# Kernel tuning notes

Measured on AMD Instinct MI355X. Metric: run time of the kernel, lower is better.

Reference implementation:

```python
import jax, jax.numpy as jnp
import numpy as np

EPS = 1e-8

def _div(a, b, eps=EPS):
    # torch: a / (b*(b>eps) + (b<=eps)*eps)
    return a / jnp.where(b > eps, b, eps)

def _cos_lastdim(a, b, eps=EPS):
    # F.cosine_similarity(a, b, dim=-1): dot / (max(|a|,eps)*max(|b|,eps))
    dot = jnp.sum(a * b, axis=-1)
    na = jnp.sqrt(jnp.sum(a * a, axis=-1))
    nb = jnp.sqrt(jnp.sum(b * b, axis=-1))
    return dot / (jnp.maximum(na, eps) * jnp.maximum(nb, eps))

def _full_matching(q1, q2, w):
    # q1,q2: [b,s,h]; w: [p,h] -> [b,s,p]
    q1w = q1[:, :, None, :] * w            # [b,s,p,h]
    q2w = q2[:, :, None, :] * w
    return _cos_lastdim(q1w, q2w)

def _max_pool_matching(q1, q2, w, eps=EPS):
    # q1: [b,s1,h]; q2: [b,s2,h]; w: [p,h] -> [b,s1,p]
    q1w = q1[:, :, None, :] * w            # [b,s1,p,h]
    q2w = q2[:, :, None, :] * w            # [b,s2,p,h]
    dots = jnp.einsum('biph,bjph->bijp', q1w, q2w)   # [b,s1,s2,p]
    n1 = jnp.maximum(jnp.sqrt(jnp.sum(q1w * q1w, -1)), eps)  # [b,s1,p]
    n2 = jnp.maximum(jnp.sqrt(jnp.sum(q2w * q2w, -1)), eps)  # [b,s2,p]
    cos = dots / (n1[:, :, None, :] * n2[:, None, :, :])
    return jnp.max(cos, axis=2)            # max over s2

def _attention(q1, q2):
    # cosine attention matrix [b,s1,s2]
    n1 = jnp.sqrt(jnp.sum(q1 * q1, -1, keepdims=True))           # [b,s1,1]
    n2 = jnp.sqrt(jnp.sum(q2 * q2, -1, keepdims=True))           # [b,s2,1]
    mol = jnp.einsum('bih,bjh->bij', q1, q2)
    return _div(mol, n1 * n2.transpose(0, 2, 1))

def setup_inputs() -> dict:
    key = jax.random.key(0)
    k1, k2, k3 = jax.random.split(key, 3)
    q1_batch = jax.random.normal(k1, (16, 128, 512), dtype=jnp.float32)
    q2_batch = jax.random.normal(k2, (16, 192, 512), dtype=jnp.float32)
    W = jax.random.normal(k3, (8, 4, 256), dtype=jnp.float32)
    return {"q1_batch": q1_batch, "q2_batch": q2_batch, "W": W}

def reference(q1_batch, q2_batch, W):
    half = q1_batch.shape[-1] // 2
    s1 = q1_batch.shape[1]
    q1_fw, q1_bw = q1_batch[..., :half], q1_batch[..., half:]
    q2_fw, q2_bw = q2_batch[..., :half], q2_batch[..., half:]

    # 1) full matching against q2 last (fw) / first (bw) state
    q2_last = jnp.broadcast_to(q2_fw[:, -1:, :], q1_fw.shape)
    q2_first = jnp.broadcast_to(q2_bw[:, :1, :], q1_bw.shape)
    full_fw = _full_matching(q1_fw, q2_last, W[0])
    full_bw = _full_matching(q1_bw, q2_first, W[1])

    # 2) max-pool matching
    max_fw = _max_pool_matching(q1_fw, q2_fw, W[2])
    max_bw = _max_pool_matching(q1_bw, q2_bw, W[3])

    # 3) attentive matching
    att_fw = _attention(q1_fw, q2_fw)   # [b,s1,s2]
    att_bw = _attention(q1_bw, q2_bw)
    attened_q2_fw = att_fw[:, :, :, None] * q2_fw[:, None, :, :]  # [b,s1,s2,h]
    attened_q2_bw = att_bw[:, :, :, None] * q2_bw[:, None, :, :]
    mean_fw = _div(attened_q2_fw.sum(axis=2), att_fw.sum(axis=2, keepdims=True))
    mean_bw = _div(attened_q2_bw.sum(axis=2), att_bw.sum(axis=2, keepdims=True))
    att_match_fw = _full_matching(q1_fw, mean_fw, W[4])
    att_match_bw = _full_matching(q1_bw, mean_bw, W[5])

    # 4) max-attentive matching
    maxatt_q2_fw = jnp.max(attened_q2_fw, axis=2)  # [b,s1,h]
    maxatt_q2_bw = jnp.max(attened_q2_bw, axis=2)
    maxatt_fw = _full_matching(q1_fw, maxatt_q2_fw, W[6])
    maxatt_bw = _full_matching(q1_bw, maxatt_q2_bw, W[7])

    return jnp.concatenate(
        [full_fw, full_bw, max_fw, max_bw,
         att_match_fw, att_match_bw, maxatt_fw, maxatt_bw], axis=-1)
```

## Files before the change

### kernel.cpp

```cpp
#include <hip/hip_runtime.h>
#include <math.h>
#include <stdint.h>

#define NB 16
#define S1 128
#define S2 192
#define HH 256
#define PP 4
#define FULLH 512
#define EPSV 1e-8f

typedef float f32x4 __attribute__((ext_vector_type(4)));
typedef float f32x2 __attribute__((ext_vector_type(2)));
typedef short short8 __attribute__((ext_vector_type(8)));

#define WS_N2    0
#define WS_N2W   6144
#define WS_N1    30720
#define WS_N1W   34816
#define WS_Q2BF  919552
#define WS_N1X   2492416
#define WS_RVN   2541568
#define WS_Q1BF  2541696

__device__ __forceinline__ float dot4(const float4& a, const float4& b) {
    return a.x * b.x + a.y * b.y + a.z * b.z + a.w * b.w;
}

__device__ __forceinline__ float vdot4(const f32x4& a, const f32x4& b) {
    return a.x * b.x + a.y * b.y + a.z * b.z + a.w * b.w;
}

__device__ __forceinline__ uint16_t f2bf(float x) {
    union { float f; uint32_t u; } a;
    a.f = x;
    uint32_t r = a.u + 0x7FFF + ((a.u >> 16) & 1);
    return (uint16_t)(r >> 16);
}

__device__ __forceinline__ uint32_t pk2(float a, float b) {
    return (uint32_t)f2bf(a) | ((uint32_t)f2bf(b) << 16);
}

template<int N>
__device__ __forceinline__ void wave_reduce_sum_n(float* v) {
#pragma unroll
    for (int m = 1; m < 64; m <<= 1) {
#pragma unroll
        for (int i = 0; i < N; i++) v[i] += __shfl_xor(v[i], m, 64);
    }
}

__global__ __launch_bounds__(256) void norms_kernel(const float* __restrict__ q1,
                                                    const float* __restrict__ q2,
                                                    const float* __restrict__ W,
                                                    float* __restrict__ ws) {
    const int NQ2 = 2 * NB * S2;
    const int NQ1 = 2 * NB * S1;
    int gwid = (int)((blockIdx.x * blockDim.x + threadIdx.x) >> 6);
    int lane = threadIdx.x & 63;
    if (gwid >= NQ2 + NQ1) return;

    int h0 = lane * 4;
    int sg = lane >> 3;
    int khalf = (lane >> 1) & 3;
    int elo = (lane & 1) * 4;

    if (gwid < NQ2) {
        int d = gwid / (NB * S2);
        int rem = gwid - d * (NB * S2);
        int b_ = rem / S2;
        int j_ = rem - b_ * S2;
        int db = d * NB + b_;
        const float* row = q2 + ((size_t)(b_ * S2 + j_)) * FULLH + d * HH;
        float4 v = *reinterpret_cast<const float4*>(row + h0);
        const float* wmax = W + (size_t)(2 + d) * PP * HH;

        float s[5];
        s[0] = dot4(v, v);
#pragma unroll
        for (int p = 0; p < PP; p++) {
            float4 wv = *reinterpret_cast<const float4*>(wmax + p * HH + h0);
            float4 t;
            t.x = v.x * wv.x; t.y = v.y * wv.y; t.z = v.z * wv.z; t.w = v.w * wv.w;
            s[1 + p] = dot4(t, t);
        }
        wave_reduce_sum_n<5>(s);
        int nidx = db * S2 + j_;
        if (lane == 0) {
            ws[WS_N2 + nidx] = sqrtf(s[0]);
#pragma unroll
            for (int p = 0; p < PP; p++)
                ws[WS_N2W + (size_t)nidx * PP + p] = sqrtf(s[1 + p]);
        }

        if ((d == 0 && j_ == S2 - 1) || (d == 1 && j_ == 0)) {
            float e[4];
#pragma unroll
            for (int p = 0; p < PP; p++) {
                float4 wv = *reinterpret_cast<const float4*>(W + ((size_t)d * PP + p) * HH + h0);
                float4 t;
                t.x = v.x * wv.x; t.y = v.y * wv.y; t.z = v.z * wv.z; t.w = v.w * wv.w;
                e[p] = dot4(t, t);
            }
            wave_reduce_sum_n<4>(e);
            if (lane == 0) {
#pragma unroll
                for (int p = 0; p < PP; p++)
                    ws[WS_RVN + db * 4 + p] = sqrtf(e[p]);
            }
        }

        uint2 pk;
        pk.x = pk2(v.x, v.y);
        pk.y = pk2(v.z, v.w);
        {
            uint16_t* q2bf = (uint16_t*)(ws + WS_Q2BF) + (size_t)db * (S2 * HH);
            int jt = j_ >> 4, jcol = j_ & 15;
            size_t off = ((size_t)(jt * 8 + sg) * 64 + (khalf << 4) + jcol) * 8 + elo;
            *reinterpret_cast<uint2*>(q2bf + off) = pk;
        }
    } else {
        int idx = gwid - NQ2;
        int d = idx >> 11;
        int b = (idx >> 7) & 15;
        int i = idx & 127;
        int db = d * NB + b;
        const float* row = q1 + ((size_t)(b * S1 + i)) * FULLH + d * HH;
        float4 v = *reinterpret_cast<const float4*>(row + h0);

        int banks[4] = {2 + d, d, 4 + d, 6 + d};
        float s[17];
        float4 y[4];
        s[0] = dot4(v, v);
#pragma unroll
        for (int t = 0; t < 4; t++) {
#pragma unroll
            for (int p = 0; p < PP; p++) {
                float4 wv = *reinterpret_cast<const float4*>(
                    W + ((size_t)banks[t] * PP + p) * HH + h0);
                float4 tv;
                tv.x = v.x * wv.x; tv.y = v.y * wv.y;
                tv.z = v.z * wv.z; tv.w = v.w * wv.w;
                s[1 + t * 4 + p] = dot4(tv, tv);
                if (t == 0) {
                    y[p].x = tv.x * wv.x; y[p].y = tv.y * wv.y;
                    y[p].z = tv.z * wv.z; y[p].w = tv.w * wv.w;
                }
            }
        }
        wave_reduce_sum_n<17>(s);
        if (lane == 0) {
            ws[WS_N1 + idx] = sqrtf(s[0]);
#pragma unroll
            for (int p = 0; p < PP; p++)
                ws[WS_N1W + (size_t)idx * PP + p] = sqrtf(s[1 + p]);
#pragma unroll
            for (int t = 0; t < 3; t++)
#pragma unroll
                for (int p = 0; p < PP; p++)
                    ws[WS_N1X + (size_t)idx * 12 + t * 4 + p] = sqrtf(s[5 + t * 4 + p]);
        }

        uint16_t* q1b5 = (uint16_t*)(ws + WS_Q1BF) + (size_t)db * 163840;
        int itile = i >> 4, icol = i & 15;
        size_t slot = (size_t)((khalf << 4) + icol) * 8 + elo;
        {
            uint2 pk;
            pk.x = pk2(v.x, v.y);
            pk.y = pk2(v.z, v.w);
            size_t so = ((size_t)(0 * 8 + itile) * 8 + sg) * 512 + slot;
            *reinterpret_cast<uint2*>(q1b5 + so) = pk;
        }
#pragma unroll
        for (int p = 0; p < PP; p++) {
            uint2 pk;
            pk.x = pk2(y[p].x, y[p].y);
            pk.y = pk2(y[p].z, y[p].w);
            size_t so = ((size_t)((p + 1) * 8 + itile) * 8 + sg) * 512 + slot;
            *reinterpret_cast<uint2*>(q1b5 + so) = pk;
        }
    }
}

__global__ __launch_bounds__(256) void sapply_kernel(const float* __restrict__ q1,
                                                     const float* __restrict__ q2,
                                                     const float* __restrict__ W,
                                                     const float* __restrict__ ws,
                                                     float* __restrict__ out) {
    __shared__ float att_s[S2][8];
    __shared__ float satt_s[4][8];
    __shared__ float mc_s[4][8][4];
    __shared__ float lds_c[4][8][HH];

    int bid = blockIdx.x;
    int xcd = bid & 7;
    int rest = bid >> 3;
    int db = xcd + 8 * (rest & 3);
    int it8 = rest >> 2;
    int d = db >> 4;
    int b = db & 15;
    int itile = it8 >> 1;
    int half = it8 & 1;

    int tid = threadIdx.x;
    int w = tid >> 6;
    int lane = tid & 63;
    int h0 = lane * 4;

    const float* q2b = q2 + (size_t)b * S2 * FULLH + d * HH;

    {
        int jq = w;
        const uint16_t* q2bfp = (const uint16_t*)(ws + WS_Q2BF) + (size_t)db * (S2 * HH);
        const uint16_t* q1bfp = (const uint16_t*)(ws + WS_Q1BF) + (size_t)db * 163840;

        f32x4 acc[5][3];
#pragma unroll
        for (int v = 0; v < 5; v++)
#pragma unroll
            for (int jt_i = 0; jt_i < 3; jt_i++) acc[v][jt_i] = (f32x4){0.f, 0.f, 0.f, 0.f};

#pragma unroll
        for (int kc = 0; kc < 4; kc++) {
            short8 Bf[3][2];
#pragma unroll
            for (int jt_i = 0; jt_i < 3; jt_i++)
#pragma unroll
                for (int sl = 0; sl < 2; sl++)
                    Bf[jt_i][sl] = *reinterpret_cast<const short8*>(
                        q2bfp + ((size_t)((jq * 3 + jt_i) * 8 + kc * 2 + sl) * 64 + lane) * 8);
#pragma unroll
            for (int v = 0; v < 5; v++) {
                short8 A0 = *reinterpret_cast<const short8*>(
                    q1bfp + ((size_t)(v * 8 + itile) * 8 + kc * 2 + 0) * 512 + lane * 8);
                short8 A1 = *reinterpret_cast<const short8*>(
                    q1bfp + ((size_t)(v * 8 + itile) * 8 + kc * 2 + 1) * 512 + lane * 8);
#pragma unroll
                for (int jt_i = 0; jt_i < 3; jt_i++) {
                    acc[v][jt_i] = __builtin_amdgcn_mfma_f32_16x16x32_bf16(A0, Bf[jt_i][0], acc[v][jt_i], 0, 0, 0);
                    acc[v][jt_i] = __builtin_amdgcn_mfma_f32_16x16x32_bf16(A1, Bf[jt_i][1], acc[v][jt_i], 0, 0, 0);
                }
            }
        }

        int lhi = lane >> 4;
        int lcol = lane & 15;
        bool keep = (lhi >> 1) == half;
        int ii0 = (lhi & 1) * 4;
        int nbase = db * S2;
        int q1b_ = db * S1 + itile * 16 + lhi * 4;

        float n1v[4], n1wc[4][4];
#pragma unroll
        for (int rr = 0; rr < 4; rr++) {
            n1v[rr] = ws[WS_N1 + q1b_ + rr];
#pragma unroll
            for (int p = 0; p < 4; p++)
                n1wc[rr][p] = fmaxf(ws[WS_N1W + (size_t)(q1b_ + rr) * 4 + p], EPSV);
        }

        float satt_acc[4] = {0.f, 0.f, 0.f, 0.f};
        float mc_acc[4][4];
#pragma unroll
        for (int p = 0; p < 4; p++)
#pragma unroll
            for (int rr = 0; rr < 4; rr++) mc_acc[p][rr] = -INFINITY;

#pragma unroll
        for (int jt_i = 0; jt_i < 3; jt_i++) {
            int j = (jq * 3 + jt_i) * 16 + lcol;
            float n2 = ws[WS_N2 + nbase + j];
            float avv[4];
#pragma unroll
            for (int rr = 0; rr < 4; rr++) {
                float den = n1v[rr] * n2;
                avv[rr] = acc[0][jt_i][rr] / (den > EPSV ? den : EPSV);
                satt_acc[rr] += avv[rr];
            }
            if (keep) {
                float4 av;
                av.x = avv[0]; av.y = avv[1]; av.z = avv[2]; av.w = avv[3];
                *reinterpret_cast<float4*>(&att_s[j][ii0]) = av;
            }
#pragma unroll
            for (int p = 0; p < 4; p++) {
                float n2wv = fmaxf(ws[WS_N2W + (size_t)(nbase + j) * 4 + p], EPSV);
#pragma unroll
                for (int rr = 0; rr < 4; rr++) {
                    float cosv = acc[p + 1][jt_i][rr] / (n1wc[rr][p] * n2wv);
                    mc_acc[p][rr] = fmaxf(mc_acc[p][rr], cosv);
                }
            }
        }

#pragma unroll
        for (int m = 1; m < 16; m <<= 1) {
#pragma unroll
            for (int rr = 0; rr < 4; rr++) satt_acc[rr] += __shfl_xor(satt_acc[rr], m, 64);
#pragma unroll
            for (int p = 0; p < 4; p++)
#pragma unroll
                for (int rr = 0; rr < 4; rr++)
                    mc_acc[p][rr] = fmaxf(mc_acc[p][rr], __shfl_xor(mc_acc[p][rr], m, 64));
        }
        if (keep && lcol == 0) {
#pragma unroll
            for (int rr = 0; rr < 4; rr++) {
                satt_s[jq][ii0 + rr] = satt_acc[rr];
#pragma unroll
                for (int p = 0; p < 4; p++)
                    mc_s[jq][ii0 + rr][p] = mc_acc[p][rr];
            }
        }
    }
    __syncthreads();

    {
        int j0 = w * 48;
        f32x4 macc[8], mx[8];
#pragma unroll
        for (int ii = 0; ii < 8; ii++) {
            macc[ii] = (f32x4){0.f, 0.f, 0.f, 0.f};
            mx[ii] = (f32x4){-INFINITY, -INFINITY, -INFINITY, -INFINITY};
        }

#pragma unroll 4
        for (int jj = 0; jj < 48; jj++) {
            int j = j0 + jj;
            f32x4 qv = *reinterpret_cast<const f32x4*>(q2b + (size_t)j * FULLH + h0);
            f32x4 a03 = *reinterpret_cast<const f32x4*>(&att_s[j][0]);
            f32x4 a47 = *reinterpret_cast<const f32x4*>(&att_s[j][4]);
            float av[8] = {a03.x, a03.y, a03.z, a03.w, a47.x, a47.y, a47.z, a47.w};
#pragma unroll
            for (int ii = 0; ii < 8; ii++) {
                f32x4 ab = (f32x4){av[ii], av[ii], av[ii], av[ii]};
                macc[ii] = __builtin_elementwise_fma(ab, qv, macc[ii]);
                mx[ii] = __builtin_elementwise_max(mx[ii], ab * qv);
            }
        }

#pragma unroll
        for (int ii = 0; ii < 8; ii++)
            *reinterpret_cast<f32x4*>(&lds_c[w][ii][h0]) = macc[ii];
        __syncthreads();

        int il0 = w * 2;
        int i0 = it8 * 8 + il0;
        f32x4 cm0 = (f32x4){0.f, 0.f, 0.f, 0.f};
        f32x4 cm1 = (f32x4){0.f, 0.f, 0.f, 0.f};
#pragma unroll
        for (int wp = 0; wp < 4; wp++) {
            cm0 += *reinterpret_cast<const f32x4*>(&lds_c[wp][il0][h0]);
            cm1 += *reinterpret_cast<const f32x4*>(&lds_c[wp][il0 + 1][h0]);
        }
        __syncthreads();

#pragma unroll
        for (int ii = 0; ii < 8; ii++)
            *reinterpret_cast<f32x4*>(&lds_c[w][ii][h0]) = mx[ii];
        __syncthreads();

        f32x4 cx0 = (f32x4){-INFINITY, -INFINITY, -INFINITY, -INFINITY};
        f32x4 cx1 = (f32x4){-INFINITY, -INFINITY, -INFINITY, -INFINITY};
#pragma unroll
        for (int wp = 0; wp < 4; wp++) {
            cx0 = __builtin_elementwise_max(cx0, *reinterpret_cast<const f32x4*>(&lds_c[wp][il0][h0]));
            cx1 = __builtin_elementwise_max(cx1, *reinterpret_cast<const f32x4*>(&lds_c[wp][il0 + 1][h0]));
        }

        float satt0 = satt_s[0][il0] + satt_s[1][il0] + satt_s[2][il0] + satt_s[3][il0];
        float satt1 = satt_s[0][il0 + 1] + satt_s[1][il0 + 1] +
                      satt_s[2][il0 + 1] + satt_s[3][il0 + 1];
        float sden0 = satt0 > EPSV ? satt0 : EPSV;
        float sden1 = satt1 > EPSV ? satt1 : EPSV;

        if (lane < 8) {
            int iw = il0 + (lane >> 2);
            int p = lane & 3;
            float m = fmaxf(fmaxf(mc_s[0][iw][p], mc_s[1][iw][p]),
                            fmaxf(mc_s[2][iw][p], mc_s[3][iw][p]));
            out[((size_t)(b * S1 + it8 * 8 + iw)) * 32 + 8 + 4 * d + p] = m;
        }

        f32x4 mean0 = cm0 * (1.0f / sden0);
        f32x4 mean1 = cm1 * (1.0f / sden1);
        f32x4 rv = *reinterpret_cast<const f32x4*>(
            q2b + (d == 0 ? (size_t)(S2 - 1) * FULLH : (size_t)0) + h0);
        f32x4 q1v0 = *reinterpret_cast<const f32x4*>(
            q1 + ((size_t)(b * S1 + i0)) * FULLH + d * HH + h0);
        f32x4 q1v1 = *reinterpret_cast<const f32x4*>(
            q1 + ((size_t)(b * S1 + i0 + 1)) * FULLH + d * HH + h0);

        f32x4 q1rv0 = q1v0 * rv, q1me0 = q1v0 * mean0, me20 = mean0 * mean0;
        f32x4 q1mx0 = q1v0 * cx0, mx20 = cx0 * cx0;
        f32x4 q1rv1 = q1v1 * rv, q1me1 = q1v1 * mean1, me21 = mean1 * mean1;
        f32x4 q1mx1 = q1v1 * cx1, mx21 = cx1 * cx1;

        float s[40];
#pragma unroll
        for (int p = 0; p < 4; p++) {
            f32x4 wf = *reinterpret_cast<const f32x4*>(W + ((size_t)d * PP + p) * HH + h0);
            f32x4 wa = *reinterpret_cast<const f32x4*>(W + ((size_t)(4 + d) * PP + p) * HH + h0);
            f32x4 wm = *reinterpret_cast<const f32x4*>(W + ((size_t)(6 + d) * PP + p) * HH + h0);
            f32x4 w2f = wf * wf, w2a = wa * wa, w2m = wm * wm;
            s[p * 5 + 0] = vdot4(q1rv0, w2f);
            s[p * 5 + 1] = vdot4(q1me0, w2a);
            s[p * 5 + 2] = vdot4(me20, w2a);
            s[p * 5 + 3] = vdot4(q1mx0, w2m);
            s[p * 5 + 4] = vdot4(mx20, w2m);
            s[20 + p * 5 + 0] = vdot4(q1rv1, w2f);
            s[20 + p * 5 + 1] = vdot4(q1me1, w2a);
            s[20 + p * 5 + 2] = vdot4(me21, w2a);
            s[20 + p * 5 + 3] = vdot4(q1mx1, w2m);
            s[20 + p * 5 + 4] = vdot4(mx21, w2m);
        }
        wave_reduce_sum_n<40>(s);

        if (lane == 0) {
#pragma unroll
            for (int ii = 0; ii < 2; ii++) {
                int i = i0 + ii;
                int qi = db * S1 + i;
                size_t obase = ((size_t)(b * S1 + i)) * 32;
                const float* nx = ws + WS_N1X + (size_t)qi * 12;
#pragma unroll
                for (int p = 0; p < 4; p++) {
                    float nf = fmaxf(nx[p], EPSV);
                    float na = fmaxf(nx[4 + p], EPSV);
                    float nm = fmaxf(nx[8 + p], EPSV);
                    float rvn = fmaxf(ws[WS_RVN + db * 4 + p], EPSV);
                    const float* sp = s + ii * 20 + p * 5;
                    out[obase + 0 + 4 * d + p] = sp[0] / (nf * rvn);
                    out[obase + 16 + 4 * d + p] = sp[1] / (na * fmaxf(sqrtf(sp[2]), EPSV));
                    out[obase + 24 + 4 * d + p] = sp[3] / (nm * fmaxf(sqrtf(sp[4]), EPSV));
                }
            }
        }
    }
}

extern "C" void kernel_launch(void* const* d_in, const int* in_sizes, int n_in,
                              void* d_out, int out_size, void* d_ws, size_t ws_size,
                              hipStream_t stream) {
    const float* q1 = (const float*)d_in[0];
    const float* q2 = (const float*)d_in[1];
    const float* W = (const float*)d_in[2];
    float* out = (float*)d_out;
    float* ws = (float*)d_ws;

    int nrows = 2 * NB * S2 + 2 * NB * S1;
    int nblocks_norm = (nrows * 64 + 255) / 256;
    norms_kernel<<<dim3(nblocks_norm), dim3(256), 0, stream>>>(q1, q2, W, ws);

    sapply_kernel<<<dim3(512), dim3(256), 0, stream>>>(q1, q2, W, ws, out);
}
```

Baseline: 57.66 us.

## Split attended-q2 accumulation by row half and j half to cut LDS reduction

Each of the four waves used to accumulate all 8 rows over a quarter of s2 and then reduce through one shared buffer in two rounds. Now each wave handles 4 rows over half of s2, and the partial sums and maxes go into separate LDS buffers that are reduced in a single round. This removes two barriers and halves the cross-wave reduction reads and register accumulators. In exchange, each q2 row is loaded by two waves instead of one, which doubles global or L2 traffic in that loop.

```diff
diff --git a/kernel.cpp b/kernel.cpp
--- a/kernel.cpp
+++ b/kernel.cpp
@@ -191,7 +191,8 @@
     __shared__ float att_s[S2][8];
     __shared__ float satt_s[4][8];
     __shared__ float mc_s[4][8][4];
-    __shared__ float lds_c[4][8][HH];
+    __shared__ float lds_m[2][8][HH];
+    __shared__ float lds_x[2][8][HH];
 
     int bid = blockIdx.x;
     int xcd = bid & 7;
@@ -317,23 +318,26 @@
     __syncthreads();
 
     {
-        int j0 = w * 48;
-        f32x4 macc[8], mx[8];
-#pragma unroll
-        for (int ii = 0; ii < 8; ii++) {
+        int ihalf = w >> 1;
+        int jhalf = w & 1;
+        int iiB = ihalf * 4;
+        int j0 = jhalf * 96;
+
+        f32x4 macc[4], mx[4];
+#pragma unroll
+        for (int ii = 0; ii < 4; ii++) {
             macc[ii] = (f32x4){0.f, 0.f, 0.f, 0.f};
             mx[ii] = (f32x4){-INFINITY, -INFINITY, -INFINITY, -INFINITY};
         }
 
-#pragma unroll 4
-        for (int jj = 0; jj < 48; jj++) {
+#pragma unroll 8
+        for (int jj = 0; jj < 96; jj++) {
             int j = j0 + jj;
             f32x4 qv = *reinterpret_cast<const f32x4*>(q2b + (size_t)j * FULLH + h0);
-            f32x4 a03 = *reinterpret_cast<const f32x4*>(&att_s[j][0]);
-            f32x4 a47 = *reinterpret_cast<const f32x4*>(&att_s[j][4]);
-            float av[8] = {a03.x, a03.y, a03.z, a03.w, a47.x, a47.y, a47.z, a47.w};
-#pragma unroll
-            for (int ii = 0; ii < 8; ii++) {
+            f32x4 a4 = *reinterpret_cast<const f32x4*>(&att_s[j][iiB]);
+            float av[4] = {a4.x, a4.y, a4.z, a4.w};
+#pragma unroll
+            for (int ii = 0; ii < 4; ii++) {
                 f32x4 ab = (f32x4){av[ii], av[ii], av[ii], av[ii]};
                 macc[ii] = __builtin_elementwise_fma(ab, qv, macc[ii]);
                 mx[ii] = __builtin_elementwise_max(mx[ii], ab * qv);
@@ -341,33 +345,24 @@
         }
 
 #pragma unroll
-        for (int ii = 0; ii < 8; ii++)
-            *reinterpret_cast<f32x4*>(&lds_c[w][ii][h0]) = macc[ii];
+        for (int ii = 0; ii < 4; ii++) {
+            *reinterpret_cast<f32x4*>(&lds_m[jhalf][iiB + ii][h0]) = macc[ii];
+            *reinterpret_cast<f32x4*>(&lds_x[jhalf][iiB + ii][h0]) = mx[ii];
+        }
         __syncthreads();
 
         int il0 = w * 2;
         int i0 = it8 * 8 + il0;
-        f32x4 cm0 = (f32x4){0.f, 0.f, 0.f, 0.f};
-        f32x4 cm1 = (f32x4){0.f, 0.f, 0.f, 0.f};
-#pragma unroll
-        for (int wp = 0; wp < 4; wp++) {
-            cm0 += *reinterpret_cast<const f32x4*>(&lds_c[wp][il0][h0]);
-            cm1 += *reinterpret_cast<const f32x4*>(&lds_c[wp][il0 + 1][h0]);
-        }
-        __syncthreads();
-
-#pragma unroll
-        for (int ii = 0; ii < 8; ii++)
-            *reinterpret_cast<f32x4*>(&lds_c[w][ii][h0]) = mx[ii];
-        __syncthreads();
-
-        f32x4 cx0 = (f32x4){-INFINITY, -INFINITY, -INFINITY, -INFINITY};
-        f32x4 cx1 = (f32x4){-INFINITY, -INFINITY, -INFINITY, -INFINITY};
-#pragma unroll
-        for (int wp = 0; wp < 4; wp++) {
-            cx0 = __builtin_elementwise_max(cx0, *reinterpret_cast<const f32x4*>(&lds_c[wp][il0][h0]));
-            cx1 = __builtin_elementwise_max(cx1, *reinterpret_cast<const f32x4*>(&lds_c[wp][il0 + 1][h0]));
-        }
+        f32x4 cm0 = *reinterpret_cast<const f32x4*>(&lds_m[0][il0][h0]) +
+                    *reinterpret_cast<const f32x4*>(&lds_m[1][il0][h0]);
+        f32x4 cm1 = *reinterpret_cast<const f32x4*>(&lds_m[0][il0 + 1][h0]) +
+                    *reinterpret_cast<const f32x4*>(&lds_m[1][il0 + 1][h0]);
+        f32x4 cx0 = __builtin_elementwise_max(
+            *reinterpret_cast<const f32x4*>(&lds_x[0][il0][h0]),
+            *reinterpret_cast<const f32x4*>(&lds_x[1][il0][h0]));
+        f32x4 cx1 = __builtin_elementwise_max(
+            *reinterpret_cast<const f32x4*>(&lds_x[0][il0 + 1][h0]),
+            *reinterpret_cast<const f32x4*>(&lds_x[1][il0 + 1][h0]));
 
         float satt0 = satt_s[0][il0] + satt_s[1][il0] + satt_s[2][il0] + satt_s[3][il0];
         float satt1 = satt_s[0][il0 + 1] + satt_s[1][il0 + 1] +
```

New measurement: 68.20 us. 18.3% more time.
